# Performance work log

Hardware: AMD Instinct MI355X
Metric: run time of the kernel (lower is better)

Reference implementation:

```python
import jax, jax.numpy as jnp
import numpy as np

MODEL_DIM = 1024
N_Q_HEADS = 16
N_GROUPS = 4
KV_PER_Q = N_Q_HEADS // N_GROUPS        # 4
HEAD_DIM = MODEL_DIM // N_Q_HEADS       # 64
KV_HEAD_DIM = MODEL_DIM // KV_PER_Q     # 256 (per-group K/V total width = N_GROUPS*HEAD_DIM)
ROPE_THETA = 50000.0


def rope_cos_sin(seq_len, dim, dtype):
    # standard RoPE tables: [S, dim]
    inv_freq = 1.0 / (ROPE_THETA ** (jnp.arange(0, dim, 2, dtype=jnp.float32) / dim))
    freqs = jnp.arange(seq_len, dtype=jnp.float32)[:, None] * inv_freq[None, :]  # [S, dim/2]
    emb = jnp.concatenate([freqs, freqs], axis=-1)                               # [S, dim]
    return jnp.cos(emb).astype(dtype), jnp.sin(emb).astype(dtype)


def rotate_half(x):
    h = x.shape[-1] // 2
    return jnp.concatenate([-x[..., h:], x[..., :h]], axis=-1)


def setup_inputs() -> dict:
    key = jax.random.key(0)
    k0, k1, k2, k3, k4 = jax.random.split(key, 5)
    B, S = 2, 2048
    qkv_out = MODEL_DIM + 2 * KV_HEAD_DIM  # 1536
    s_in = 1.0 / np.sqrt(MODEL_DIM)
    return {
        "x": jax.random.normal(k0, (B, S, MODEL_DIM), jnp.float32),
        "W_qkv": jax.random.normal(k1, (MODEL_DIM, qkv_out), jnp.float32) * s_in,
        "b_qkv": jnp.zeros((qkv_out,), jnp.float32),
        "W_out": jax.random.normal(k2, (MODEL_DIM, MODEL_DIM), jnp.float32) * s_in,
        "b_out": jnp.zeros((MODEL_DIM,), jnp.float32),
    }


def reference(x, W_qkv, b_qkv, W_out, b_out):
    B, S, _ = x.shape
    fused = x @ W_qkv + b_qkv  # [B,S,MODEL_DIM + 2*KV_HEAD_DIM]
    q, k, v = jnp.split(fused, [MODEL_DIM, MODEL_DIM + KV_HEAD_DIM], axis=-1)

    # [B,S,(NH HD)] -> [B,NH,S,HD]
    q = q.reshape(B, S, N_Q_HEADS, HEAD_DIM).transpose(0, 2, 1, 3)
    k = k.reshape(B, S, N_GROUPS, HEAD_DIM).transpose(0, 2, 1, 3)
    v = v.reshape(B, S, N_GROUPS, HEAD_DIM).transpose(0, 2, 1, 3)

    cos, sin = rope_cos_sin(S, HEAD_DIM, x.dtype)  # [S,HD]
    cos = cos[None, None]                          # [1,1,S,HD]
    sin = sin[None, None]
    q = q * cos + rotate_half(q) * sin
    k = k * cos + rotate_half(k) * sin

    # GQA without materializing duplicated heads: group queries [B,G,R,S,HD]
    qg = q.reshape(B, N_GROUPS, KV_PER_Q, S, HEAD_DIM)
    scale = 1.0 / np.sqrt(HEAD_DIM)
    scores = jnp.einsum('bgrsh,bgth->bgrst', qg, k) * scale  # [B,G,R,S,S]
    causal = jnp.tril(jnp.ones((S, S), bool))
    scores = jnp.where(causal, scores, jnp.finfo(scores.dtype).min)
    probs = jax.nn.softmax(scores, axis=-1)
    out = jnp.einsum('bgrst,bgth->bgrsh', probs, v)          # [B,G,R,S,HD]

    # [B,G,R,S,HD] -> [B,S,MODEL_DIM]  (head index = g*R + r, matching duplicate_heads)
    out = out.reshape(B, N_Q_HEADS, S, HEAD_DIM).transpose(0, 2, 1, 3).reshape(B, S, MODEL_DIM)
    return out @ W_out + b_out
```

## Files before the change

kernel.cpp:

```cpp
#include <hip/hip_runtime.h>
#include <hip/hip_bf16.h>

typedef __attribute__((ext_vector_type(8))) short short8;
typedef __attribute__((ext_vector_type(4))) float f32x4;

__device__ __forceinline__ short tobf(float f) {
  __hip_bfloat16 h = __float2bfloat16(f);
  return *reinterpret_cast<short*>(&h);
}
__device__ __forceinline__ float frombf(short s) {
  unsigned u = ((unsigned)(unsigned short)s) << 16;
  return __uint_as_float(u);
}

__device__ __forceinline__ int swz(int row) { return (row ^ (row >> 3)) & 7; }

#define GLDS16(gp, lp) __builtin_amdgcn_global_load_lds( \
    (__attribute__((address_space(1))) void*)(gp),       \
    (__attribute__((address_space(3))) void*)(lp), 16, 0, 0)

__device__ __forceinline__ float exp2raw(float x) {
  float r;
  asm("v_exp_f32 %0, %1" : "=v"(r) : "v"(x));
  return r;
}
__device__ __forceinline__ unsigned cvtpk(float lo, float hi) {
  unsigned r;
  asm("v_cvt_pk_bf16_f32 %0, %1, %2" : "=v"(r) : "v"(lo), "v"(hi));
  return r;
}

#define QSCALE 0.18033688011112042f

__global__ __launch_bounds__(256) void prep_k(
    const float* __restrict__ x, short* __restrict__ xb,
    const float* __restrict__ Wqkv, short* __restrict__ WqkvT,
    const float* __restrict__ Wout, short* __restrict__ WoutT,
    float* __restrict__ cost, float* __restrict__ sint) {
  __shared__ float t[64][65];
  const int bx = blockIdx.x, tid = threadIdx.x;
  if (bx < 1024) {
    int base = bx * 4096 + tid * 4;
#pragma unroll
    for (int rep = 0; rep < 4; ++rep) {
      int i = base + rep * 1024;
      float4 v = *(const float4*)(x + i);
      *(short4*)(xb + i) = make_short4(tobf(v.x), tobf(v.y), tobf(v.z), tobf(v.w));
    }
  } else if (bx < 1664) {
    const float* in;
    short* out;
    int C, bb;
    if (bx < 1408) { in = Wqkv; out = WqkvT; C = 1536; bb = bx - 1024; }
    else           { in = Wout; out = WoutT; C = 1024; bb = bx - 1408; }
    const int R = 1024;
    int nc = C >> 6;
    int br = bb / nc, bc = bb % nc;
    int lr = tid >> 6, lc = tid & 63;
#pragma unroll
    for (int j = 0; j < 16; ++j) {
      int r = j * 4 + lr;
      t[r][lc] = in[(size_t)(br * 64 + r) * C + bc * 64 + lc];
    }
    __syncthreads();
#pragma unroll
    for (int j = 0; j < 16; ++j) {
      int r = j * 4 + lr;
      out[(size_t)(bc * 64 + r) * R + br * 64 + lc] = tobf(t[lc][r]);
    }
  } else {
    int t2 = (bx - 1664) * 256 + tid;
    int s = t2 >> 5, f = t2 & 31;
    float inv = __expf(-(float)f * (logf(50000.0f) / 32.0f));
    float a = (float)s * inv;
    cost[t2] = cosf(a);
    sint[t2] = sinf(a);
  }
}

template <int MODE>
__global__ __launch_bounds__(256) void gemm_k(
    const short* __restrict__ A, const short* __restrict__ Bt,
    const float* __restrict__ bias, void* __restrict__ Cout,
    short* __restrict__ vT,
    int M, int N, int K,
    const float* __restrict__ cost, const float* __restrict__ sint) {
  __shared__ short As[128 * 64];
  __shared__ short Bs[64 * 64];
  const int ntile = N >> 6;
  const int bm = blockIdx.x / ntile, bn = blockIdx.x % ntile;
  const int tid = threadIdx.x, w = tid >> 6, l = tid & 63;
  const int c = l & 15, g = l >> 4;
  const int m0 = bm * 128, n0 = bn * 64;

  f32x4 acc[2][4] = {};

  for (int k0 = 0; k0 < K; k0 += 64) {
#pragma unroll
    for (int j = 0; j < 4; ++j) {
      int rb = j * 32 + w * 8;
      int row = rb + (l >> 3);
      int colel = ((l & 7) ^ swz(row)) * 8;
      GLDS16(A + (size_t)(m0 + row) * K + k0 + colel, &As[rb * 64]);
      if (j < 2) GLDS16(Bt + (size_t)(n0 + row) * K + k0 + colel, &Bs[rb * 64]);
    }
    __syncthreads();
#pragma unroll
    for (int kk = 0; kk < 2; ++kk) {
      short8 af[2], bf[4];
#pragma unroll
      for (int mi = 0; mi < 2; ++mi) {
        int row = w * 32 + mi * 16 + c;
        af[mi] = *(const short8*)&As[row * 64 + ((kk * 4 + g) ^ swz(row)) * 8];
      }
#pragma unroll
      for (int ni = 0; ni < 4; ++ni) {
        int row = ni * 16 + c;
        bf[ni] = *(const short8*)&Bs[row * 64 + ((kk * 4 + g) ^ swz(row)) * 8];
      }
#pragma unroll
      for (int mi = 0; mi < 2; ++mi)
#pragma unroll
        for (int ni = 0; ni < 4; ++ni)
          acc[mi][ni] = __builtin_amdgcn_mfma_f32_16x16x32_bf16(af[mi], bf[ni], acc[mi][ni], 0, 0, 0);
    }
    __syncthreads();
  }

  if (MODE == 0 && n0 >= 1280) {
    const int hg = (n0 - 1280) >> 6;
#pragma unroll
    for (int mi = 0; mi < 2; ++mi) {
      int m0r = m0 + w * 32 + mi * 16 + g * 4;
      int b = m0r >> 11, s = m0r & 2047;
#pragma unroll
      for (int ni = 0; ni < 4; ++ni) {
        int d = ni * 16 + c;
        float bs = bias[n0 + d];
        short4 o;
        o.x = tobf(acc[mi][ni][0] + bs);
        o.y = tobf(acc[mi][ni][1] + bs);
        o.z = tobf(acc[mi][ni][2] + bs);
        o.w = tobf(acc[mi][ni][3] + bs);
        *(short4*)&vT[(size_t)((b * 4 + hg) * 64 + d) * 2048 + s] = o;
      }
    }
    return;
  }

#pragma unroll
  for (int mi = 0; mi < 2; ++mi)
#pragma unroll
    for (int r = 0; r < 4; ++r) {
      int m = m0 + w * 32 + mi * 16 + g * 4 + r;
      int s = m & 2047;
#pragma unroll
      for (int ni = 0; ni < 4; ++ni) {
        int n = n0 + ni * 16 + c;
        float v = acc[mi][ni][r] + bias[n];
        if (MODE == 0) {
          int d = n & 63, f = d & 31;
          float cs = cost[s * 32 + f], sn = sint[s * 32 + f];
          float partner = acc[mi][ni ^ 2][r] + bias[n ^ 32];
          v = (d < 32) ? (v * cs - partner * sn) : (v * cs + partner * sn);
          if (n < 1024) v *= QSCALE;
          ((short*)Cout)[(size_t)m * N + n] = tobf(v);
        } else {
          ((float*)Cout)[(size_t)m * N + n] = v;
        }
      }
    }
}

__global__ __launch_bounds__(512) void attn_k(const short* __restrict__ qkv,
                                              const short* __restrict__ vT,
                                              short* __restrict__ pacc,
                                              float* __restrict__ plrun) {
  __shared__ short Ks6[6][64 * 64];
  __shared__ short Vt6[6][64 * 64];
  __shared__ short Ps[8][16 * 64];

  const int bx = blockIdx.x;
  const int bh = bx & 31;
  const int rest = bx >> 5;
  const int p = rest & 3;
  const int half = rest >> 2;
  const int qtB = 7 - p, qtA = p;
  const int sB = 32 - 4 * p;
  const int start = half * 18;
  const int end = start + 18;
  const int b = bh >> 4, h = bh & 15, hg = h >> 2;
  const int tid = threadIdx.x, w = tid >> 6, l = tid & 63;
  const int c = l & 15, g = l >> 4;
  const size_t rowbase = (size_t)(b * 2048) * 1536;

  const int srow = w * 8 + (l >> 3);
  const int scol = ((l & 7) ^ swz(srow)) * 8;
  const size_t koff = (size_t)srow * 1536 + scol;
  const size_t voff = (size_t)srow * 2048 + scol;
  const int ldsoff = (w * 8) * 64;
  const short* kbase = qkv + rowbase + 1024 + hg * 64;
  const short* vbase_p = vT + (size_t)((b * 4 + hg) * 64) * 2048;

#define KTOF(i) (((i) < sB) ? (i) : ((i) - sB))

#pragma unroll
  for (int t = 0; t < 4; ++t) {
    int idx = start + t;
    int kt0 = KTOF(idx);
    int bf_ = idx % 6;
    GLDS16(kbase + (size_t)kt0 * 98304 + koff, &Ks6[bf_][ldsoff]);
    GLDS16(vbase_p + kt0 * 64 + voff, &Vt6[bf_][ldsoff]);
  }
  asm volatile("s_waitcnt vmcnt(4)" ::: "memory");
  __builtin_amdgcn_s_barrier();
  __builtin_amdgcn_sched_barrier(0);

  f32x4 acco[2][4] = {};
  float lrun[2] = {0.f, 0.f};
  short* Pw = &Ps[w][0];
  short8 aq[2][2];

#pragma unroll
  for (int set = 0; set < 2; ++set)
#pragma unroll
    for (int kk = 0; kk < 2; ++kk)
      aq[set][kk] = *(const short8*)(qkv + rowbase +
          (size_t)(qtB * 256 + w * 32 + set * 16 + c) * 1536 + h * 64 + kk * 32 + g * 8);

#define CORE(qtc, TI)                                                           \
  {                                                                             \
    const int kt_ = KTOF(TI);                                                   \
    const int bf_ = (TI) % 6;                                                   \
    short8 bk[2][4];                                                            \
    _Pragma("unroll") for (int kk = 0; kk < 2; ++kk)                            \
      _Pragma("unroll") for (int nb = 0; nb < 4; ++nb) {                        \
        int row = nb * 16 + c;                                                  \
        bk[kk][nb] = *(const short8*)&Ks6[bf_][row * 64 + ((kk * 4 + g) ^ swz(row)) * 8]; \
      }                                                                         \
    f32x4 sfr[2][4] = {};                                                       \
    __builtin_amdgcn_s_setprio(1);                                              \
    _Pragma("unroll") for (int set = 0; set < 2; ++set)                         \
      _Pragma("unroll") for (int kk = 0; kk < 2; ++kk)                          \
        _Pragma("unroll") for (int nb = 0; nb < 4; ++nb)                        \
          sfr[set][nb] = __builtin_amdgcn_mfma_f32_16x16x32_bf16(               \
              bk[kk][nb], aq[set][kk], sfr[set][nb], 0, 0, 0);                  \
    __builtin_amdgcn_s_setprio(0);                                              \
    short8 bv[2][4];                                                            \
    _Pragma("unroll") for (int kk = 0; kk < 2; ++kk)                            \
      _Pragma("unroll") for (int nb = 0; nb < 4; ++nb) {                        \
        int row = nb * 16 + c;                                                  \
        bv[kk][nb] = *(const short8*)&Vt6[bf_][row * 64 + ((kk * 4 + g) ^ swz(row)) * 8]; \
      }                                                                         \
    if (kt_ >= 4 * (qtc)) {           \
      _Pragma("unroll") for (int set = 0; set < 2; ++set) {                     \
        int qg = (qtc)*256 + w * 32 + set * 16 + c;                             \
        _Pragma("unroll") for (int nb = 0; nb < 4; ++nb)                        \
          _Pragma("unroll") for (int r = 0; r < 4; ++r)                         \
            if (kt_ * 64 + nb * 16 + g * 4 + r > qg) sfr[set][nb][r] = -1e30f;  \
      }                                                                         \
    }                                                                           \
    _Pragma("unroll") for (int set = 0; set < 2; ++set) {                       \
      float rsn[4];                                                             \
      _Pragma("unroll") for (int nb = 0; nb < 4; ++nb) {                        \
        float p0 = exp2raw(sfr[set][nb][0]);                                    \
        float p1 = exp2raw(sfr[set][nb][1]);                                    \
        float p2 = exp2raw(sfr[set][nb][2]);                                    \
        float p3 = exp2raw(sfr[set][nb][3]);                                    \
        sfr[set][nb][0] = p0; sfr[set][nb][1] = p1;                             \
        sfr[set][nb][2] = p2; sfr[set][nb][3] = p3;                             \
        rsn[nb] = (p0 + p1) + (p2 + p3);                                        \
      }                                                                         \
      lrun[set] += (rsn[0] + rsn[1]) + (rsn[2] + rsn[3]);                       \
      _Pragma("unroll") for (int nb = 0; nb < 4; ++nb) {                        \
        unsigned d0 = cvtpk(sfr[set][nb][0], sfr[set][nb][1]);                  \
        unsigned d1 = cvtpk(sfr[set][nb][2], sfr[set][nb][3]);                  \
        int pslot = (nb * 2 + (g >> 1)) ^ swz(c);                               \
        int2 pq2 = make_int2((int)d0, (int)d1);                                 \
        *(int2*)&Pw[c * 64 + pslot * 8 + (g & 1) * 4] = pq2;                    \
      }                                                                         \
      __builtin_amdgcn_s_setprio(1);                                            \
      _Pragma("unroll") for (int kk = 0; kk < 2; ++kk) {                        \
        short8 ap = *(const short8*)&Pw[c * 64 + (((kk * 4 + g) ^ swz(c)) * 8)];\
        _Pragma("unroll") for (int nb = 0; nb < 4; ++nb)                        \
          acco[set][nb] = __builtin_amdgcn_mfma_f32_16x16x32_bf16(              \
              ap, bv[kk][nb], acco[set][nb], 0, 0, 0);                          \
      }                                                                         \
      __builtin_amdgcn_s_setprio(0);                                            \
    }                                                                           \
  }

#define SUPER(qtc)                                                              \
  {                                                                             \
    const bool pf_ = (i + 4 < end);                                             \
    if (pf_) {                                                                  \
      int ta = KTOF(i + 4), tb = KTOF(i + 5);                                   \
      int ba = (i + 4) % 6, bb2 = (i + 5) % 6;                                  \
      GLDS16(kbase + (size_t)ta * 98304 + koff, &Ks6[ba][ldsoff]);              \
      GLDS16(vbase_p + ta * 64 + voff, &Vt6[ba][ldsoff]);                       \
      GLDS16(kbase + (size_t)tb * 98304 + koff, &Ks6[bb2][ldsoff]);             \
      GLDS16(vbase_p + tb * 64 + voff, &Vt6[bb2][ldsoff]);                      \
    }                                                                           \
    CORE(qtc, i);                                                               \
    CORE(qtc, i + 1);                                                           \
    if (pf_) asm volatile("s_waitcnt vmcnt(4)" ::: "memory");                   \
    else     asm volatile("s_waitcnt vmcnt(0)" ::: "memory");                   \
    __builtin_amdgcn_s_barrier();                                               \
    __builtin_amdgcn_sched_barrier(0);                                          \
  }

#define STORE_PARTIAL(slot)                                                     \
  {                                                                             \
    int sidx = ((bh * 4 + p) * 2 + half) * 2 + (slot);                          \
    size_t pb = (size_t)sidx * 16384;                                           \
    _Pragma("unroll") for (int set = 0; set < 2; ++set) {                       \
      _Pragma("unroll") for (int nb = 0; nb < 4; ++nb)                          \
        _Pragma("unroll") for (int r = 0; r < 4; ++r) {                         \
          int row = w * 32 + set * 16 + g * 4 + r;                              \
          pacc[pb + row * 64 + nb * 16 + c] = tobf(acco[set][nb][r]);           \
          acco[set][nb][r] = 0.f;                                               \
        }                                                                       \
      float lr_ = lrun[set];                                                    \
      lr_ += __shfl_xor(lr_, 16, 64);                                           \
      lr_ += __shfl_xor(lr_, 32, 64);          \
      if (g == 0) plrun[sidx * 256 + w * 32 + set * 16 + c] = lr_;              \
      lrun[set] = 0.f;                                                          \
    }                                                                           \
  }

  int i = start;
  const int endB = (end < sB) ? end : sB;
  for (; i < endB; i += 2) SUPER(qtB);
  STORE_PARTIAL(0);

#pragma unroll
  for (int set = 0; set < 2; ++set)
#pragma unroll
    for (int kk = 0; kk < 2; ++kk)
      aq[set][kk] = *(const short8*)(qkv + rowbase +
          (size_t)(qtA * 256 + w * 32 + set * 16 + c) * 1536 + h * 64 + kk * 32 + g * 8);

  for (; i < end; i += 2) SUPER(qtA);
  STORE_PARTIAL(1);

#undef CORE
#undef SUPER
#undef STORE_PARTIAL
#undef KTOF
}

__global__ __launch_bounds__(256) void combine_k(const short* __restrict__ pacc,
                                                 const float* __restrict__ plrun,
                                                 short* __restrict__ attnb) {
  int e = blockIdx.x * 256 + threadIdx.x;
  int d8 = e & 7;
  int t = e >> 3;
  int row = t & 255;
  int t2 = t >> 8;
  int qt = t2 & 7;
  int bh = t2 >> 3;
  int p = (qt < 7 - qt) ? qt : 7 - qt;
  int slot = (qt >= 4) ? 0 : 1;
  float acc[8] = {};
  float lsum = 0.f;
#pragma unroll
  for (int half = 0; half < 2; ++half) {
    int sidx = ((bh * 4 + p) * 2 + half) * 2 + slot;
    short8 a = *(const short8*)(pacc + (size_t)sidx * 16384 + row * 64 + d8 * 8);
#pragma unroll
    for (int k = 0; k < 8; ++k) acc[k] += frombf(a[k]);
    lsum += plrun[sidx * 256 + row];
  }
  float li = 1.0f / lsum;
  int b = bh >> 4, h = bh & 15;
  int m = b * 2048 + qt * 256 + row;
  int n = h * 64 + d8 * 8;
  short8 o;
#pragma unroll
  for (int k = 0; k < 8; ++k) o[k] = tobf(acc[k] * li);
  *(short8*)(attnb + (size_t)m * 1024 + n) = o;
}

extern "C" void kernel_launch(void* const* d_in, const int* in_sizes, int n_in,
                              void* d_out, int out_size, void* d_ws, size_t ws_size,
                              hipStream_t stream) {
  const float* x    = (const float*)d_in[0];
  const float* Wqkv = (const float*)d_in[1];
  const float* bqkv = (const float*)d_in[2];
  const float* Wout = (const float*)d_in[3];
  const float* bout = (const float*)d_in[4];

  char* ws = (char*)d_ws;
  short* pacc  = (short*)(ws + 0);
  short* xb    = (short*)(ws + 0);
  short* WqkvT = (short*)(ws + 8388608);
  float* cost  = (float*)(ws + 11534336);
  float* sint  = (float*)(ws + 11796480);
  short* WoutT = (short*)(ws + 33554432);
  short* qkvb  = (short*)(ws + 35651584);
  short* attnb = (short*)(ws + 35651584);
  short* vTb   = (short*)(ws + 48234496);
  float* plrun = (float*)(ws + 50331648);

  prep_k<<<1920, 256, 0, stream>>>(x, xb, Wqkv, WqkvT, Wout, WoutT, cost, sint);
  gemm_k<0><<<768, 256, 0, stream>>>(xb, WqkvT, bqkv, (void*)qkvb, vTb, 4096, 1536, 1024, cost, sint);
  attn_k<<<256, 512, 0, stream>>>(qkvb, vTb, pacc, plrun);
  combine_k<<<2048, 256, 0, stream>>>(pacc, plrun, attnb);
  gemm_k<1><<<512, 256, 0, stream>>>(attnb, WoutT, bout, d_out, nullptr, 4096, 1024, 1024, cost, sint);
}
```

Baseline: 89.09 us.

## Enlarge attention query tile to 512 rows and split KV into quarters

```diff
diff --git a/kernel.cpp b/kernel.cpp
--- a/kernel.cpp
+++ b/kernel.cpp
@@ -183,12 +183,12 @@
   const int bx = blockIdx.x;
   const int bh = bx & 31;
   const int rest = bx >> 5;
-  const int p = rest & 3;
-  const int half = rest >> 2;
-  const int qtB = 7 - p, qtA = p;
-  const int sB = 32 - 4 * p;
-  const int start = half * 18;
-  const int end = start + 18;
+  const int p = rest & 1;
+  const int quarter = rest >> 1;
+  const int qtB = 3 - p, qtA = p;
+  const int sB = 8 * (qtB + 1);
+  const int start = quarter * 10;
+  const int end = start + 10;
   const int b = bh >> 4, h = bh & 15, hg = h >> 2;
   const int tid = threadIdx.x, w = tid >> 6, l = tid & 63;
   const int c = l & 15, g = l >> 4;
@@ -216,65 +216,59 @@
   __builtin_amdgcn_s_barrier();
   __builtin_amdgcn_sched_barrier(0);
 
-  f32x4 acco[2][4] = {};
-  float lrun[2] = {0.f, 0.f};
+  f32x4 acco[4][4] = {};
+  float lrun[4] = {0.f, 0.f, 0.f, 0.f};
   short* Pw = &Ps[w][0];
-  short8 aq[2][2];
-
-#pragma unroll
-  for (int set = 0; set < 2; ++set)
+  short8 aq[4][2];
+
+#pragma unroll
+  for (int set = 0; set < 4; ++set)
 #pragma unroll
     for (int kk = 0; kk < 2; ++kk)
       aq[set][kk] = *(const short8*)(qkv + rowbase +
-          (size_t)(qtB * 256 + w * 32 + set * 16 + c) * 1536 + h * 64 + kk * 32 + g * 8);
+          (size_t)(qtB * 512 + w * 64 + set * 16 + c) * 1536 + h * 64 + kk * 32 + g * 8);
 
 #define CORE(qtc, TI)                                                           \
   {                                                                             \
     const int kt_ = KTOF(TI);                                                   \
     const int bf_ = (TI) % 6;                                                   \
-    short8 bk[2][4];                                                            \
+    short8 bk[2][4], bv[2][4];                                                  \
     _Pragma("unroll") for (int kk = 0; kk < 2; ++kk)                            \
       _Pragma("unroll") for (int nb = 0; nb < 4; ++nb) {                        \
         int row = nb * 16 + c;                                                  \
-        bk[kk][nb] = *(const short8*)&Ks6[bf_][row * 64 + ((kk * 4 + g) ^ swz(row)) * 8]; \
+        int cs_ = ((kk * 4 + g) ^ swz(row)) * 8;                                \
+        bk[kk][nb] = *(const short8*)&Ks6[bf_][row * 64 + cs_];                 \
+        bv[kk][nb] = *(const short8*)&Vt6[bf_][row * 64 + cs_];                 \
       }                                                                         \
-    f32x4 sfr[2][4] = {};                                                       \
-    __builtin_amdgcn_s_setprio(1);                                              \
-    _Pragma("unroll") for (int set = 0; set < 2; ++set)                         \
+    const bool diag_ = (kt_ >= 8 * (qtc));                                      \
+    _Pragma("unroll") for (int set = 0; set < 4; ++set) {                       \
+      f32x4 sfr[4] = {};                                                        \
+      __builtin_amdgcn_s_setprio(1);                                            \
       _Pragma("unroll") for (int kk = 0; kk < 2; ++kk)                          \
         _Pragma("unroll") for (int nb = 0; nb < 4; ++nb)                        \
-          sfr[set][nb] = __builtin_amdgcn_mfma_f32_16x16x32_bf16(               \
-              bk[kk][nb], aq[set][kk], sfr[set][nb], 0, 0, 0);                  \
-    __builtin_amdgcn_s_setprio(0);                                              \
-    short8 bv[2][4];                                                            \
-    _Pragma("unroll") for (int kk = 0; kk < 2; ++kk)                            \
-      _Pragma("unroll") for (int nb = 0; nb < 4; ++nb) {                        \
-        int row = nb * 16 + c;                                                  \
-        bv[kk][nb] = *(const short8*)&Vt6[bf_][row * 64 + ((kk * 4 + g) ^ swz(row)) * 8]; \
-      }                                                                         \
-    if (kt_ >= 4 * (qtc)) {           \
-      _Pragma("unroll") for (int set = 0; set < 2; ++set) {                     \
-        int qg = (qtc)*256 + w * 32 + set * 16 + c;                             \
+          sfr[nb] = __builtin_amdgcn_mfma_f32_16x16x32_bf16(                    \
+              bk[kk][nb], aq[set][kk], sfr[nb], 0, 0, 0);                       \
+      __builtin_amdgcn_s_setprio(0);                                            \
+      if (diag_) {                                                              \
+        int qg = (qtc)*512 + w * 64 + set * 16 + c;                             \
         _Pragma("unroll") for (int nb = 0; nb < 4; ++nb)                        \
           _Pragma("unroll") for (int r = 0; r < 4; ++r)                         \
-            if (kt_ * 64 + nb * 16 + g * 4 + r > qg) sfr[set][nb][r] = -1e30f;  \
+            if (kt_ * 64 + nb * 16 + g * 4 + r > qg) sfr[nb][r] = -1e30f;       \
       }                                                                         \
-    }                                                                           \
-    _Pragma("unroll") for (int set = 0; set < 2; ++set) {                       \
       float rsn[4];                                                             \
       _Pragma("unroll") for (int nb = 0; nb < 4; ++nb) {                        \
-        float p0 = exp2raw(sfr[set][nb][0]);                                    \
-        float p1 = exp2raw(sfr[set][nb][1]);                                    \
-        float p2 = exp2raw(sfr[set][nb][2]);                                    \
-        float p3 = exp2raw(sfr[set][nb][3]);                                    \
-        sfr[set][nb][0] = p0; sfr[set][nb][1] = p1;                             \
-        sfr[set][nb][2] = p2; sfr[set][nb][3] = p3;                             \
+        float p0 = exp2raw(sfr[nb][0]);                                         \
+        float p1 = exp2raw(sfr[nb][1]);                                         \
+        float p2 = exp2raw(sfr[nb][2]);                                         \
+        float p3 = exp2raw(sfr[nb][3]);                                         \
+        sfr[nb][0] = p0; sfr[nb][1] = p1;                                       \
+        sfr[nb][2] = p2; sfr[nb][3] = p3;                                       \
         rsn[nb] = (p0 + p1) + (p2 + p3);                                        \
       }                                                                         \
       lrun[set] += (rsn[0] + rsn[1]) + (rsn[2] + rsn[3]);                       \
       _Pragma("unroll") for (int nb = 0; nb < 4; ++nb) {                        \
-        unsigned d0 = cvtpk(sfr[set][nb][0], sfr[set][nb][1]);                  \
-        unsigned d1 = cvtpk(sfr[set][nb][2], sfr[set][nb][3]);                  \
+        unsigned d0 = cvtpk(sfr[nb][0], sfr[nb][1]);                            \
+        unsigned d1 = cvtpk(sfr[nb][2], sfr[nb][3]);                            \
         int pslot = (nb * 2 + (g >> 1)) ^ swz(c);                               \
         int2 pq2 = make_int2((int)d0, (int)d1);                                 \
         *(int2*)&Pw[c * 64 + pslot * 8 + (g & 1) * 4] = pq2;                    \
@@ -311,19 +305,19 @@
 
 #define STORE_PARTIAL(slot)                                                     \
   {                                                                             \
-    int sidx = ((bh * 4 + p) * 2 + half) * 2 + (slot);                          \
-    size_t pb = (size_t)sidx * 16384;                                           \
-    _Pragma("unroll") for (int set = 0; set < 2; ++set) {                       \
+    int sidx = ((bh * 2 + p) * 4 + quarter) * 2 + (slot);                       \
+    size_t pb = (size_t)sidx * 32768;                                           \
+    _Pragma("unroll") for (int set = 0; set < 4; ++set) {                       \
       _Pragma("unroll") for (int nb = 0; nb < 4; ++nb)                          \
         _Pragma("unroll") for (int r = 0; r < 4; ++r) {                         \
-          int row = w * 32 + set * 16 + g * 4 + r;                              \
+          int row = w * 64 + set * 16 + g * 4 + r;                              \
           pacc[pb + row * 64 + nb * 16 + c] = tobf(acco[set][nb][r]);           \
           acco[set][nb][r] = 0.f;                                               \
         }                                                                       \
       float lr_ = lrun[set];                                                    \
       lr_ += __shfl_xor(lr_, 16, 64);                                           \
       lr_ += __shfl_xor(lr_, 32, 64);          \
-      if (g == 0) plrun[sidx * 256 + w * 32 + set * 16 + c] = lr_;              \
+      if (g == 0) plrun[sidx * 512 + w * 64 + set * 16 + c] = lr_;              \
       lrun[set] = 0.f;                                                          \
     }                                                                           \
   }
@@ -334,11 +328,11 @@
   STORE_PARTIAL(0);
 
 #pragma unroll
-  for (int set = 0; set < 2; ++set)
+  for (int set = 0; set < 4; ++set)
 #pragma unroll
     for (int kk = 0; kk < 2; ++kk)
       aq[set][kk] = *(const short8*)(qkv + rowbase +
-          (size_t)(qtA * 256 + w * 32 + set * 16 + c) * 1536 + h * 64 + kk * 32 + g * 8);
+          (size_t)(qtA * 512 + w * 64 + set * 16 + c) * 1536 + h * 64 + kk * 32 + g * 8);
 
   for (; i < end; i += 2) SUPER(qtA);
   STORE_PARTIAL(1);
@@ -355,25 +349,25 @@
   int e = blockIdx.x * 256 + threadIdx.x;
   int d8 = e & 7;
   int t = e >> 3;
-  int row = t & 255;
-  int t2 = t >> 8;
-  int qt = t2 & 7;
-  int bh = t2 >> 3;
-  int p = (qt < 7 - qt) ? qt : 7 - qt;
-  int slot = (qt >= 4) ? 0 : 1;
+  int row = t & 511;
+  int t2 = t >> 9;
+  int qt = t2 & 3;
+  int bh = t2 >> 2;
+  int pair = (qt == 3 || qt == 0) ? 0 : 1;
+  int slot = (qt >= 2) ? 0 : 1;
   float acc[8] = {};
   float lsum = 0.f;
 #pragma unroll
-  for (int half = 0; half < 2; ++half) {
-    int sidx = ((bh * 4 + p) * 2 + half) * 2 + slot;
-    short8 a = *(const short8*)(pacc + (size_t)sidx * 16384 + row * 64 + d8 * 8);
+  for (int q = 0; q < 4; ++q) {
+    int sidx = ((bh * 2 + pair) * 4 + q) * 2 + slot;
+    short8 a = *(const short8*)(pacc + (size_t)sidx * 32768 + row * 64 + d8 * 8);
 #pragma unroll
     for (int k = 0; k < 8; ++k) acc[k] += frombf(a[k]);
-    lsum += plrun[sidx * 256 + row];
+    lsum += plrun[sidx * 512 + row];
   }
   float li = 1.0f / lsum;
   int b = bh >> 4, h = bh & 15;
-  int m = b * 2048 + qt * 256 + row;
+  int m = b * 2048 + qt * 512 + row;
   int n = h * 64 + d8 * 8;
   short8 o;
 #pragma unroll
```

Result: slower. 138.4 us (+55.3%).

## Double-buffer GEMM LDS tiles to overlap global loads with MFMA

Applied to the files above, without the earlier changes.

```diff
diff --git a/kernel.cpp b/kernel.cpp
--- a/kernel.cpp
+++ b/kernel.cpp
@@ -85,38 +85,57 @@
     short* __restrict__ vT,
     int M, int N, int K,
     const float* __restrict__ cost, const float* __restrict__ sint) {
-  __shared__ short As[128 * 64];
-  __shared__ short Bs[64 * 64];
+  __shared__ short As[2][128 * 64];
+  __shared__ short Bs[2][64 * 64];
   const int ntile = N >> 6;
   const int bm = blockIdx.x / ntile, bn = blockIdx.x % ntile;
   const int tid = threadIdx.x, w = tid >> 6, l = tid & 63;
   const int c = l & 15, g = l >> 4;
   const int m0 = bm * 128, n0 = bn * 64;
 
+  const int jrow = l >> 3;
+  const int jcol = l & 7;
+
   f32x4 acc[2][4] = {};
 
-  for (int k0 = 0; k0 < K; k0 += 64) {
-#pragma unroll
-    for (int j = 0; j < 4; ++j) {
-      int rb = j * 32 + w * 8;
-      int row = rb + (l >> 3);
-      int colel = ((l & 7) ^ swz(row)) * 8;
-      GLDS16(A + (size_t)(m0 + row) * K + k0 + colel, &As[rb * 64]);
-      if (j < 2) GLDS16(Bt + (size_t)(n0 + row) * K + k0 + colel, &Bs[rb * 64]);
-    }
-    __syncthreads();
+#pragma unroll
+  for (int j = 0; j < 4; ++j) {
+    int rb = j * 32 + w * 8;
+    int row = rb + jrow;
+    int colel = (jcol ^ swz(row)) * 8;
+    GLDS16(A + (size_t)(m0 + row) * K + colel, &As[0][rb * 64]);
+    if (j < 2) GLDS16(Bt + (size_t)(n0 + row) * K + colel, &Bs[0][rb * 64]);
+  }
+  asm volatile("s_waitcnt vmcnt(0)" ::: "memory");
+  __builtin_amdgcn_s_barrier();
+  __builtin_amdgcn_sched_barrier(0);
+
+  const int niter = K >> 6;
+  for (int it = 0; it < niter; ++it) {
+    const int cur = it & 1, nxt = cur ^ 1;
+    const int k0n = (it + 1) << 6;
+    if (it + 1 < niter) {
+#pragma unroll
+      for (int j = 0; j < 4; ++j) {
+        int rb = j * 32 + w * 8;
+        int row = rb + jrow;
+        int colel = (jcol ^ swz(row)) * 8;
+        GLDS16(A + (size_t)(m0 + row) * K + k0n + colel, &As[nxt][rb * 64]);
+        if (j < 2) GLDS16(Bt + (size_t)(n0 + row) * K + k0n + colel, &Bs[nxt][rb * 64]);
+      }
+    }
 #pragma unroll
     for (int kk = 0; kk < 2; ++kk) {
       short8 af[2], bf[4];
 #pragma unroll
       for (int mi = 0; mi < 2; ++mi) {
         int row = w * 32 + mi * 16 + c;
-        af[mi] = *(const short8*)&As[row * 64 + ((kk * 4 + g) ^ swz(row)) * 8];
+        af[mi] = *(const short8*)&As[cur][row * 64 + ((kk * 4 + g) ^ swz(row)) * 8];
       }
 #pragma unroll
       for (int ni = 0; ni < 4; ++ni) {
         int row = ni * 16 + c;
-        bf[ni] = *(const short8*)&Bs[row * 64 + ((kk * 4 + g) ^ swz(row)) * 8];
+        bf[ni] = *(const short8*)&Bs[cur][row * 64 + ((kk * 4 + g) ^ swz(row)) * 8];
       }
 #pragma unroll
       for (int mi = 0; mi < 2; ++mi)
@@ -124,7 +143,9 @@
         for (int ni = 0; ni < 4; ++ni)
           acc[mi][ni] = __builtin_amdgcn_mfma_f32_16x16x32_bf16(af[mi], bf[ni], acc[mi][ni], 0, 0, 0);
     }
-    __syncthreads();
+    asm volatile("s_waitcnt vmcnt(0)" ::: "memory");
+    __builtin_amdgcn_s_barrier();
+    __builtin_amdgcn_sched_barrier(0);
   }
 
   if (MODE == 0 && n0 >= 1280) {
```

Measured after the change: 88.03 us. No clear change (-1.2%).
